# Performance work log

Measured on AMD Instinct MI355X. Metric: run time of the kernel, lower is better.

Reference implementation:

```python
import jax, jax.numpy as jnp
import numpy as np

B, DIM, H, W = 4, 96, 256, 256
HEADS = 4
EPS = 1e-12

def conv1x1(x, w, b):
    # x: [b,c,h,w], w: [o,c,1,1], b: [o]
    return jnp.einsum('bchw,oc->bohw', x, w[:, :, 0, 0]) + b[None, :, None, None]

def dwconv3x3(x, w, b):
    # depthwise 3x3, w: [c,1,3,3]
    c = x.shape[1]
    y = jax.lax.conv_general_dilated(
        x, w, window_strides=(1, 1), padding='SAME',
        feature_group_count=c, dimension_numbers=('NCHW', 'OIHW', 'NCHW'))
    return y + b[None, :, None, None]

def setup_inputs() -> dict:
    key = jax.random.key(0)
    ks = jax.random.split(key, 16)
    d = DIM
    s = 0.05
    return {
        'content': jax.random.normal(ks[0], (B, d, H, W), jnp.float32),
        'style': jax.random.normal(ks[1], (B, d, H, W), jnp.float32),
        'temperature': jnp.ones((HEADS, 1, 1), jnp.float32),
        'q_w': jax.random.normal(ks[2], (d, d, 1, 1), jnp.float32) * s,
        'q_b': jax.random.normal(ks[3], (d,), jnp.float32) * s,
        'qd_w': jax.random.normal(ks[4], (d, 1, 3, 3), jnp.float32) * s,
        'qd_b': jax.random.normal(ks[5], (d,), jnp.float32) * s,
        'kv_w': jax.random.normal(ks[6], (3 * d, d, 1, 1), jnp.float32) * s,
        'kv_b': jax.random.normal(ks[7], (3 * d,), jnp.float32) * s,
        'kvd_w': jax.random.normal(ks[8], (3 * d, 1, 3, 3), jnp.float32) * s,
        'kvd_b': jax.random.normal(ks[9], (3 * d,), jnp.float32) * s,
        'ps_w': jax.random.normal(ks[10], (d, d, 1, 1), jnp.float32) * s,
        'ps_b': jax.random.normal(ks[11], (d,), jnp.float32) * s,
        'psh_w': jax.random.normal(ks[12], (d, d, 1, 1), jnp.float32) * s,
        'psh_b': jax.random.normal(ks[13], (d,), jnp.float32) * s,
    }

def _heads(x, b, h, w):
    # [b, head*c, h, w] -> [b, head, c, h*w]
    return x.reshape(b, HEADS, x.shape[1] // HEADS, h * w)

def reference(content, style, temperature, q_w, q_b, qd_w, qd_b,
              kv_w, kv_b, kvd_w, kvd_b, ps_w, ps_b, psh_w, psh_b):
    b, c, h, w = content.shape
    kv = dwconv3x3(conv1x1(style, kv_w, kv_b), kvd_w, kvd_b)
    k, v_scale, v_shift = jnp.split(kv, 3, axis=1)
    q = dwconv3x3(conv1x1(content, q_w, q_b), qd_w, qd_b)

    q = _heads(q, b, h, w)
    k = _heads(k, b, h, w)
    v_scale = _heads(v_scale, b, h, w)
    v_shift = _heads(v_shift, b, h, w)

    # L2-normalize over spatial dim (torch F.normalize eps=1e-12)
    q = q / jnp.maximum(jnp.linalg.norm(q, axis=-1, keepdims=True), EPS)
    k = k / jnp.maximum(jnp.linalg.norm(k, axis=-1, keepdims=True), EPS)

    # attn: [b, head, c, c] (channel attention, tiny)
    attn = jnp.einsum('bhcn,bhdn->bhcd', q, k) * temperature[None]
    attn = jax.nn.softmax(attn, axis=-1)

    scale = jnp.einsum('bhcd,bhdn->bhcn', attn, v_scale).reshape(b, c, h, w)
    shift = jnp.einsum('bhcd,bhdn->bhcn', attn, v_shift).reshape(b, c, h, w)

    scale = conv1x1(scale, ps_w, ps_b)
    shift = conv1x1(shift, psh_w, psh_b)
    return (scale, shift)
```

## Files before the change

### kernel.cpp

```cpp
#include <hip/hip_runtime.h>

#define NB 4
#define C 96
#define HH 256
#define WW 256
#define NPIX (HH*WW)
#define HEADS 4
#define CH 24

#define NTX2 16
#define NTY2 19
#define NTILES (NTX2*NTY2)
#define YP 296
#define QP 264
#define VP 104
#define KSPLIT 128
#define YR 24
#define YC 392
#define XTP 76

#define WS_SUMSQ_Q 0
#define WS_SUMSQ_K (WS_SUMSQ_Q + NB*C)
#define WS_GRAM    (WS_SUMSQ_K + NB*C)
#define WS_MS      (WS_GRAM + NB*HEADS*CH*CH)
#define WS_MSH     (WS_MS + NB*C*C)

#define XT_OFF_BYTES ((size_t)335872)
#define XT_BYTES   ((size_t)2*NB*NPIX*96*2)

#define F_PSQ_OFF   (XT_OFF_BYTES + XT_BYTES)
#define F_PSQ_BYTES ((size_t)NTILES*NB*192*4)
#define F_PG_OFF    (F_PSQ_OFF + F_PSQ_BYTES)
#define F_PG_BYTES  ((size_t)NTILES*NB*HEADS*1024*4)
#define F_MB_OFF    (F_PG_OFF + F_PG_BYTES)
#define F_MB_BYTES  ((size_t)2*NB*96*96*2)
#define F_WS_NEED   (F_MB_OFF + F_MB_BYTES)

#define QK_OFF    (XT_OFF_BYTES + XT_BYTES)
#define QK_BYTES  ((size_t)2*NB*96*NPIX*2)
#define VB_OFF    (QK_OFF + QK_BYTES)
#define VB_BYTES  ((size_t)NB*NPIX*96*2)
#define PG_OFF    (VB_OFF + VB_BYTES)
#define PG_BYTES  ((size_t)KSPLIT*NB*9216*4)
#define PSQ_OFF   (PG_OFF + PG_BYTES)
#define PSQ_BYTES ((size_t)4*NTILES*NB*48*4)
#define MB_OFF    (PSQ_OFF + PSQ_BYTES)
#define MB_BYTES  ((size_t)2*NB*96*96*2)
#define WB_OFF    (MB_OFF + MB_BYTES)
#define WB_BYTES  ((size_t)384*96*2)
#define WS_NEED2  (WB_OFF + WB_BYTES)

typedef short short8 __attribute__((ext_vector_type(8)));
typedef float f32x4 __attribute__((ext_vector_type(4)));
typedef float f32x16 __attribute__((ext_vector_type(16)));

__device__ __forceinline__ unsigned short f2b(float f){
  unsigned u = __float_as_uint(f);
  unsigned r = u + 0x7FFFu + ((u >> 16) & 1u);
  return (unsigned short)(r >> 16);
}
__device__ __forceinline__ float b2f(unsigned short s){
  return __uint_as_float(((unsigned)s) << 16);
}
__device__ __forceinline__ short8 pack8(float4 a, float4 b){
  short8 r;
  r[0]=(short)f2b(a.x); r[1]=(short)f2b(a.y); r[2]=(short)f2b(a.z); r[3]=(short)f2b(a.w);
  r[4]=(short)f2b(b.x); r[5]=(short)f2b(b.y); r[6]=(short)f2b(b.z); r[7]=(short)f2b(b.w);
  return r;
}

__global__ __launch_bounds__(256) void k0t(
  const float* __restrict__ content, const float* __restrict__ style,
  unsigned short* __restrict__ xt, int cm)
{
  __shared__ unsigned short Xt[96*XTP];
  const int t = threadIdx.x;
  const int n0 = blockIdx.x * 64;
  const int b = blockIdx.y, src = blockIdx.z;
  const int gyr = n0 >> 8, gxb = n0 & 255;
  const float* in = (src ? style : content) + (size_t)b*C*NPIX;
  #pragma unroll
  for (int i = 0; i < 6; ++i){
    int s = i*256 + t;
    int r = s >> 4, c4 = s & 15;
    float4 f = *(const float4*)(in + (size_t)r*NPIX + n0 + c4*4);
    unsigned lo = ((unsigned)f2b(f.y) << 16) | f2b(f.x);
    unsigned hi = ((unsigned)f2b(f.w) << 16) | f2b(f.z);
    *(uint2*)&Xt[r*XTP + c4*4] = make_uint2(lo, hi);
  }
  __syncthreads();
  unsigned* dst = (unsigned*)(xt + ((size_t)src*NB + b)*NPIX*96);
  #pragma unroll
  for (int i = 0; i < 12; ++i){
    int s = i*256 + t;
    int j = s / 48, c2 = s - j*48;
    unsigned v = ((unsigned)Xt[(c2*2+1)*XTP + j] << 16) | Xt[(c2*2)*XTP + j];
    size_t np = cm ? ((size_t)(gxb + j)*HH + gyr) : (size_t)(n0 + j);
    dst[np*48 + c2] = v;
  }
}

__global__ __launch_bounds__(256) void kwpack(
  const float* __restrict__ q_w, const float* __restrict__ kv_w,
  unsigned short* __restrict__ wb)
{
  int i = blockIdx.x*256 + threadIdx.x;
  if (i < 9216) wb[i] = f2b(q_w[i]);
  else if (i < 36864) wb[i] = f2b(kv_w[i - 9216]);
}

__global__ __launch_bounds__(512, 4) void kconv(
  const unsigned short* __restrict__ xt, const unsigned short* __restrict__ wb,
  const float* __restrict__ q_b, const float* __restrict__ qd_w, const float* __restrict__ qd_b,
  const float* __restrict__ kv_b, const float* __restrict__ kvd_w, const float* __restrict__ kvd_b,
  unsigned short* __restrict__ qk, unsigned short* __restrict__ vbs,
  unsigned short* __restrict__ vbh, float* __restrict__ psq)
{
  __shared__ unsigned short Ysh[48*YC];
  __shared__ float red[48];
  const int t = threadIdx.x, lane = t & 63, w = t >> 6;
  const int tile = blockIdx.x, b = blockIdx.y, z = blockIdx.z;
  const int txx = tile & 15, tyy = tile >> 4;
  const int gx0 = txx*16, gy0 = tyy*14;
  const unsigned short* xsrc = xt + ((size_t)((z < 2 ? 0 : 1)*NB + b))*NPIX*96;
  const int wrow0 = (z < 2) ? z*48 : 96 + (z-2)*48;
  const float* cb  = (z<2) ? q_b  + z*48           : kv_b  + (size_t)(z-2)*48;
  const float* dww = (z<2) ? qd_w + (size_t)z*48*9 : kvd_w + (size_t)(z-2)*48*9;
  const float* dwb = (z<2) ? qd_b + z*48           : kvd_b + (size_t)(z-2)*48;
  unsigned short* dst0;
  if (z < 2)      dst0 = qk  + ((size_t)(0*NB + b)*96 + (size_t)z*48)*NPIX;
  else if (z < 4) dst0 = qk  + ((size_t)(1*NB + b)*96 + (size_t)(z-2)*48)*NPIX;
  else if (z < 6) dst0 = vbs + ((size_t)b*96 + (size_t)(z-4)*48)*NPIX;
  else            dst0 = vbh + ((size_t)b*96 + (size_t)(z-6)*48)*NPIX;

  if (t < 48) red[t] = 0.f;

  const int hy = lane & 15, khalf = lane >> 4;
  const int gyh = gy0 - 1 + hy;
  short8 xf[3][3]; bool imv[3];
  const int np = (w < 2) ? 3 : 2;
  #pragma unroll
  for (int i = 0; i < 3; ++i){
    if (i >= np) break;
    int pt = w + i*8;
    int gx = gx0 - 1 + pt;
    bool im = (gx>=0) && (gx<WW) && (gyh>=0) && (gyh<HH);
    imv[i] = im;
    const unsigned short* xp = xsrc + (size_t)(im ? (gx*HH + gyh) : 0)*96 + khalf*8;
    short8 zz = {};
    #pragma unroll
    for (int kk = 0; kk < 3; ++kk){
      short8 v = *(const short8*)(xp + kk*32);
      xf[i][kk] = im ? v : zz;
    }
  }

  #pragma unroll 1
  for (int mi = 0; mi < 3; ++mi){
    const unsigned short* wp = wb + (size_t)(wrow0 + mi*16 + hy)*96 + khalf*8;
    short8 a0 = *(const short8*)(wp);
    short8 a1 = *(const short8*)(wp + 32);
    short8 a2 = *(const short8*)(wp + 64);
    float4 bv = *(const float4*)&cb[mi*16 + khalf*4];
    #pragma unroll
    for (int i = 0; i < 3; ++i){
      if (i >= np) break;
      int pt = w + i*8;
      f32x4 acc = {bv.x, bv.y, bv.z, bv.w};
      acc = __builtin_amdgcn_mfma_f32_16x16x32_bf16(a0, xf[i][0], acc, 0,0,0);
      acc = __builtin_amdgcn_mfma_f32_16x16x32_bf16(a1, xf[i][1], acc, 0,0,0);
      acc = __builtin_amdgcn_mfma_f32_16x16x32_bf16(a2, xf[i][2], acc, 0,0,0);
      #pragma unroll
      for (int r = 0; r < 4; ++r){
        int ch = mi*16 + khalf*4 + r;
        Ysh[ch*YC + hy*YR + pt] = imv[i] ? f2b(acc[r]) : (unsigned short)0;
      }
    }
  }
  __syncthreads();

  for (int sl = lane; sl < 84; sl += 64){
    int slot = w*84 + sl;
    int c = slot / 14, py = slot - (slot/14)*14;
    int gy = gy0 + py;
    if (gy < HH){
      const float* wd = dww + (size_t)c*9;
      float w00=wd[0],w01=wd[1],w02=wd[2],w10=wd[3],w11=wd[4],w12=wd[5],w20=wd[6],w21=wd[7],w22=wd[8];
      float bb = dwb[c];
      const unsigned short* yb = &Ysh[c*YC + py*YR];
      float o[16];
      #pragma unroll
      for (int half = 0; half < 2; ++half){
        float u[3][10];
        #pragma unroll
        for (int uu = 0; uu < 3; ++uu){
          const unsigned short* rp = yb + uu*YR + half*8;
          short8 s = *(const short8*)rp;
          unsigned ex = *(const unsigned*)(rp + 8);
          #pragma unroll
          for (int j = 0; j < 8; ++j) u[uu][j] = b2f((unsigned short)s[j]);
          u[uu][8] = b2f((unsigned short)(ex & 0xffffu));
          u[uu][9] = b2f((unsigned short)(ex >> 16));
        }
        #pragma unroll
        for (int j = 0; j < 8; ++j){
          float s = bb;
          s = fmaf(w00,u[0][j],s); s = fmaf(w01,u[0][j+1],s); s = fmaf(w02,u[0][j+2],s);
          s = fmaf(w10,u[1][j],s); s = fmaf(w11,u[1][j+1],s); s = fmaf(w12,u[1][j+2],s);
          s = fmaf(w20,u[2][j],s); s = fmaf(w21,u[2][j+1],s); s = fmaf(w22,u[2][j+2],s);
          o[half*8 + j] = s;
        }
      }
      unsigned short vv[16];
      if (z < 4){
        float sq = 0.f;
        #pragma unroll
        for (int j = 0; j < 16; ++j){ sq = fmaf(o[j], o[j], sq); vv[j] = f2b(o[j]); }
        atomicAdd(&red[c], sq);
      } else {
        #pragma unroll
        for (int j = 0; j < 16; ++j) vv[j] = f2b(o[j]);
      }
      unsigned short* qp = dst0 + (size_t)c*NPIX + (size_t)gy*WW + gx0;
      *(short8*)qp       = *(const short8*)&vv[0];
      *(short8*)(qp + 8) = *(const short8*)&vv[8];
    }
  }
  if (z < 4){
    __syncthreads();
    if (t < 48)
      psq[((size_t)(z*NTILES + tile)*NB + b)*48 + t] = red[t];
  }
}

__global__ __launch_bounds__(384) void kgram(
  const unsigned short* __restrict__ qk, float* __restrict__ pg)
{
  const int t = threadIdx.x, lane = t & 63, wv = t >> 6;
  const int ks = blockIdx.x, b = blockIdx.y;
  const int n0 = ks * (NPIX / KSPLIT);
  const unsigned short* qb = qk + ((size_t)(0*NB + b)*96)*NPIX;
  const unsigned short* kb = qk + ((size_t)(1*NB + b)*96)*NPIX;
  f32x4 acc[6];
  #pragma unroll
  for (int i = 0; i < 6; ++i) acc[i] = (f32x4){0.f,0.f,0.f,0.f};
  #pragma unroll 1
  for (int st = 0; st < (NPIX/KSPLIT)/32; ++st){
    int off = n0 + st*32 + (lane>>4)*8;
    short8 bf = *(const short8*)(kb + (size_t)(wv*16 + (lane&15))*NPIX + off);
    #pragma unroll
    for (int ci = 0; ci < 6; ++ci){
      short8 af = *(const short8*)(qb + (size_t)(ci*16 + (lane&15))*NPIX + off);
      acc[ci] = __builtin_amdgcn_mfma_f32_16x16x32_bf16(af, bf, acc[ci], 0,0,0);
    }
  }
  float* dst = pg + ((size_t)ks*NB + b)*9216;
  #pragma unroll
  for (int ci = 0; ci < 6; ++ci){
    #pragma unroll
    for (int r = 0; r < 4; ++r)
      dst[(ci*6 + wv)*256 + ((lane>>4)*4 + r)*16 + (lane&15)] = acc[ci][r];
  }
}

__global__ __launch_bounds__(256) void kgredN(
  const float* __restrict__ pg, const float* __restrict__ psq, float* __restrict__ ws)
{
  const int b = blockIdx.x, by = blockIdx.y, t = threadIdx.x;
  if (by < 36){
    int ci = by / 6;
    int qrow = ci*16 + (t >> 4), krow = (by - ci*6)*16 + (t & 15);
    float s = 0.f;
    for (int ks = 0; ks < KSPLIT; ++ks)
      s += pg[((size_t)ks*NB + b)*9216 + by*256 + t];
    int h = qrow / CH;
    if (krow / CH == h)
      ws[WS_GRAM + ((size_t)(b*HEADS + h)*CH + (qrow % CH))*CH + (krow % CH)] = s;
  } else {
    if (t < 192){
      int src = t / 96, c = t - (t/96)*96;
      int zz = src*2 + (c/48), cc = c - (c/48)*48;
      float s = 0.f;
      for (int tile = 0; tile < NTILES; ++tile)
        s += psq[((size_t)(zz*NTILES + tile)*NB + b)*48 + cc];
      ws[(src ? WS_SUMSQ_K : WS_SUMSQ_Q) + b*C + c] = s;
    }
  }
}

__global__ void k2_attn(
  const float* __restrict__ temp,
  const float* __restrict__ ps_w, const float* __restrict__ psh_w,
  float* __restrict__ ws, unsigned short* __restrict__ mb)
{
  const int b = blockIdx.x;
  const int t = threadIdx.x;
  __shared__ float attn[C * CH];
  __shared__ float nq[C], nk[C];
  if (t < C){
    nq[t] = fmaxf(sqrtf(ws[WS_SUMSQ_Q + b * C + t]), 1e-12f);
    nk[t] = fmaxf(sqrtf(ws[WS_SUMSQ_K + b * C + t]), 1e-12f);
  }
  __syncthreads();
  if (t < C){
    int h = t / CH;
    const float* g = ws + WS_GRAM + (((size_t)b * HEADS + h) * CH + (t % CH)) * CH;
    float tp = temp[h];
    float row[CH];
    float mx = -3.4e38f;
    #pragma unroll
    for (int d = 0; d < CH; ++d){
      row[d] = g[d] / (nq[t] * nk[h * CH + d]) * tp;
      mx = fmaxf(mx, row[d]);
    }
    float s = 0.f;
    #pragma unroll
    for (int d = 0; d < CH; ++d){ row[d] = expf(row[d] - mx); s += row[d]; }
    float inv = 1.f / s;
    #pragma unroll
    for (int d = 0; d < CH; ++d) attn[t * CH + d] = row[d] * inv;
  }
  __syncthreads();
  for (int idx = t; idx < C * C; idx += 256){
    int o = idx / C, dg = idx - o * C;
    int h = dg / CH, d = dg - h * CH;
    float s1 = 0.f, s2 = 0.f;
    #pragma unroll
    for (int c2 = 0; c2 < CH; ++c2){
      float a = attn[(h * CH + c2) * CH + d];
      s1 = fmaf(ps_w [(size_t)o * C + h * CH + c2], a, s1);
      s2 = fmaf(psh_w[(size_t)o * C + h * CH + c2], a, s2);
    }
    ws[WS_MS  + (size_t)b * C * C + idx] = s1;
    ws[WS_MSH + (size_t)b * C * C + idx] = s2;
    if (mb){
      mb[((size_t)0*NB + b)*9216 + idx] = f2b(s1);
      mb[((size_t)1*NB + b)*9216 + idx] = f2b(s2);
    }
  }
}

__global__ __launch_bounds__(512) void kMv(
  const unsigned short* __restrict__ vb, const unsigned short* __restrict__ mb,
  const float* __restrict__ bias, float* __restrict__ out)
{
  __shared__ unsigned short vS[256*VP + 32*8];
  unsigned* vS32 = (unsigned*)vS;
  const int t = threadIdx.x, lane = t & 63, w = t >> 6;
  const int b = blockIdx.y;
  const int n0 = blockIdx.x * 256;
  const unsigned short* vbase = vb + (size_t)b*96*NPIX;
  #pragma unroll
  for (int i = 0; i < 3; ++i){
    int task = i*512 + t;
    int cp = task >> 5, seg = task & 31;
    const unsigned short* r0 = vbase + (size_t)(2*cp)*NPIX + n0 + seg*8;
    short8 a  = *(const short8*)r0;
    short8 bq = *(const short8*)(r0 + NPIX);
    #pragma unroll
    for (int j = 0; j < 8; ++j){
      int px = seg*8 + j;
      unsigned d = ((unsigned)(unsigned short)bq[j] << 16) | (unsigned)(unsigned short)a[j];
      vS32[px*(VP/2) + (px>>3)*4 + cp] = d;
    }
  }
  __syncthreads();
  const unsigned short* mbb = mb + (size_t)b*9216;
  float* ob = out + (size_t)b*C*NPIX;
  #pragma unroll 1
  for (int mi = 0; mi < 6; ++mi){
    const unsigned short* mp = mbb + (size_t)(mi*16 + (lane & 15))*96 + (lane>>4)*8;
    short8 a0 = *(const short8*)(mp);
    short8 a1 = *(const short8*)(mp + 32);
    short8 a2 = *(const short8*)(mp + 64);
    float4 bv = *(const float4*)&bias[mi*16 + (lane>>4)*4];
    #pragma unroll
    for (int g = 0; g < 2; ++g){
      int px = (w*2 + g)*16 + (lane & 15);
      const unsigned short* xb = &vS[px*VP + (px>>3)*8 + (lane>>4)*8];
      f32x4 acc = {bv.x, bv.y, bv.z, bv.w};
      acc = __builtin_amdgcn_mfma_f32_16x16x32_bf16(a0, *(const short8*)(xb),    acc, 0,0,0);
      acc = __builtin_amdgcn_mfma_f32_16x16x32_bf16(a1, *(const short8*)(xb+32), acc, 0,0,0);
      acc = __builtin_amdgcn_mfma_f32_16x16x32_bf16(a2, *(const short8*)(xb+64), acc, 0,0,0);
      #pragma unroll
      for (int r = 0; r < 4; ++r)
        ob[(size_t)(mi*16 + (lane>>4)*4 + r)*NPIX + n0 + px] = acc[r];
    }
  }
}

__device__ __forceinline__ void conv48c(
  const unsigned short* __restrict__ xbase, const float* __restrict__ wmat,
  const float* __restrict__ bias, int row0,
  int gx0, int gy0, int lane, int w, unsigned short* __restrict__ Ysh)
{
  const int hy = lane & 15, khalf = lane >> 4;
  const int gy = gy0 - 1 + hy;
  short8 xf[3][3]; bool imv[3]; int np = (w < 2) ? 3 : 2;
  #pragma unroll
  for (int i = 0; i < 3; ++i){
    if (i >= np) break;
    int pt = w + i*8;
    int gx = gx0 - 1 + pt;
    bool im = (gx>=0) && (gx<WW) && (gy>=0) && (gy<HH);
    imv[i] = im;
    int n = im ? (gy*WW + gx) : 0;
    const unsigned short* xp = xbase + (size_t)n*96 + khalf*8;
    short8 z = {};
    #pragma unroll
    for (int kk = 0; kk < 3; ++kk){
      short8 v = *(const short8*)(xp + kk*32);
      xf[i][kk] = im ? v : z;
    }
  }
  #pragma unroll 1
  for (int mi = 0; mi < 3; ++mi){
    int orow = row0 + mi*16 + hy;
    const float* wp = wmat + (size_t)orow*96 + khalf*8;
    short8 a0 = pack8(*(const float4*)(wp),    *(const float4*)(wp+4));
    short8 a1 = pack8(*(const float4*)(wp+32), *(const float4*)(wp+36));
    short8 a2 = pack8(*(const float4*)(wp+64), *(const float4*)(wp+68));
    float4 bv = *(const float4*)&bias[row0 + mi*16 + khalf*4];
    #pragma unroll
    for (int i = 0; i < 3; ++i){
      if (i >= np) break;
      int pt = w + i*8;
      f32x4 acc = {bv.x, bv.y, bv.z, bv.w};
      acc = __builtin_amdgcn_mfma_f32_16x16x32_bf16(a0, xf[i][0], acc, 0,0,0);
      acc = __builtin_amdgcn_mfma_f32_16x16x32_bf16(a1, xf[i][1], acc, 0,0,0);
      acc = __builtin_amdgcn_mfma_f32_16x16x32_bf16(a2, xf[i][2], acc, 0,0,0);
      #pragma unroll
      for (int r = 0; r < 4; ++r){
        int ch = mi*16 + khalf*4 + r;
        Ysh[ch*YP + pt*16 + hy] = imv[i] ? f2b(acc[r]) : (unsigned short)0;
      }
    }
  }
}

__global__ __launch_bounds__(512, 4) void kqk(
  const unsigned short* __restrict__ xt,
  const float* __restrict__ q_w, const float* __restrict__ q_b,
  const float* __restrict__ qd_w, const float* __restrict__ qd_b,
  const float* __restrict__ kv_w, const float* __restrict__ kv_b,
  const float* __restrict__ kvd_w, const float* __restrict__ kvd_b,
  float* __restrict__ pg, float* __restrict__ psq)
{
  __shared__ unsigned short Ysh[48*YP];
  __shared__ unsigned short qS[48*QP];
  __shared__ unsigned short kT[48*QP];
  __shared__ float redq[C], redk[C];

  const int t = threadIdx.x, lane = t & 63, w = t >> 6;
  const int b = blockIdx.y, tile = blockIdx.x;
  const int txx = tile & 15, tyy = tile >> 4;
  const int gx0 = txx*16, gy0 = tyy*14;
  if (t < C){ redq[t] = 0.f; redk[t] = 0.f; }
  __syncthreads();

  const unsigned short* xc = xt + ((size_t)(0*NB + b))*NPIX*96;
  const unsigned short* xs = xt + ((size_t)(1*NB + b))*NPIX*96;

  auto dwQK = [&](const float* dww, const float* dwb, int wrow0,
                  unsigned short* dst, float* red){
    for (int slot = t; slot < 48*16; slot += 512){
      int c = slot >> 4, j = slot & 15;
      const unsigned short* yb = &Ysh[c*YP + j*16];
      float u0[16], u1[16], u2[16];
      {
        short8 s0 = *(const short8*)(yb),    s1 = *(const short8*)(yb+8);
        short8 s2 = *(const short8*)(yb+16), s3 = *(const short8*)(yb+24);
        short8 s4 = *(const short8*)(yb+32), s5 = *(const short8*)(yb+40);
        #pragma unroll
        for (int u = 0; u < 8; ++u){
          u0[u]=b2f((unsigned short)s0[u]); u0[u+8]=b2f((unsigned short)s1[u]);
          u1[u]=b2f((unsigned short)s2[u]); u1[u+8]=b2f((unsigned short)s3[u]);
          u2[u]=b2f((unsigned short)s4[u]); u2[u+8]=b2f((unsigned short)s5[u]);
        }
      }
      const float* wd = dww + (size_t)(wrow0 + c)*9;
      float w00=wd[0],w01=wd[1],w02=wd[2],w10=wd[3],w11=wd[4],w12=wd[5],w20=wd[6],w21=wd[7],w22=wd[8];
      float bb = dwb[wrow0 + c];
      unsigned short vv[16];
      float sq = 0.f;
      #pragma unroll
      for (int py = 0; py < 14; ++py){
        float s = bb;
        s = fmaf(w00,u0[py],s); s = fmaf(w10,u0[py+1],s); s = fmaf(w20,u0[py+2],s);
        s = fmaf(w01,u1[py],s); s = fmaf(w11,u1[py+1],s); s = fmaf(w21,u1[py+2],s);
        s = fmaf(w02,u2[py],s); s = fmaf(w12,u2[py+1],s); s = fmaf(w22,u2[py+2],s);
        if (gy0 + py >= HH) s = 0.f;
        sq = fmaf(s, s, sq);
        vv[py] = f2b(s);
      }
      vv[14] = 0; vv[15] = 0;
      atomicAdd(&red[wrow0 + c], sq);
      *(short8*)&dst[c*QP + j*16]     = *(short8*)&vv[0];
      *(short8*)&dst[c*QP + j*16 + 8] = *(short8*)&vv[8];
    }
  };

  auto gram = [&](int cc){
    int hl = w & 1, slice = w >> 1;
    int cl = lane & 31; bool cv = cl < CH;
    int row = hl*CH + (cv ? cl : 0);
    f32x16 g;
    #pragma unroll
    for (int r = 0; r < 16; ++r) g[r] = 0.f;
    short8 z = {};
    for (int ks = slice; ks < 16; ks += 4){
      int ko = ks*16 + (lane>>5)*8;
      short8 qa = *(const short8*)&qS[row*QP + ko];
      short8 kb = *(const short8*)&kT[row*QP + ko];
      if (!cv){ qa = z; kb = z; }
      g = __builtin_amdgcn_mfma_f32_32x32x16_bf16(qa, kb, g, 0,0,0);
    }
    float* stg = (float*)Ysh;
    if (slice != 0){
      float* dst = stg + (size_t)(hl*3 + slice - 1)*1024;
      #pragma unroll
      for (int r = 0; r < 16; ++r) dst[r*64 + lane] = g[r];
    }
    __syncthreads();
    if (slice == 0){
      const float* s0 = stg + (size_t)(hl*3 + 0)*1024;
      const float* s1 = stg + (size_t)(hl*3 + 1)*1024;
      const float* s2 = stg + (size_t)(hl*3 + 2)*1024;
      float* dst = pg + ((size_t)(tile*NB + b)*HEADS + cc*2 + hl)*1024;
      #pragma unroll
      for (int r = 0; r < 16; ++r){
        int ix = r*64 + lane;
        dst[ix] = g[r] + s0[ix] + s1[ix] + s2[ix];
      }
    }
  };

  #pragma unroll 1
  for (int cc = 0; cc < 2; ++cc){
    conv48c(xc, q_w, q_b, cc*48, gx0, gy0, lane, w, Ysh);
    __syncthreads();
    dwQK(qd_w, qd_b, cc*48, qS, redq);
    __syncthreads();
    conv48c(xs, kv_w, kv_b, cc*48, gx0, gy0, lane, w, Ysh);
    __syncthreads();
    dwQK(kvd_w, kvd_b, cc*48, kT, redk);
    __syncthreads();
    gram(cc);
    __syncthreads();
  }
  if (t < 192){
    float v = (t < 96) ? redq[t] : redk[t - 96];
    psq[(size_t)(tile*NB + b)*192 + t] = v;
  }
}

__global__ __launch_bounds__(256) void kgredF(
  const float* __restrict__ pg, const float* __restrict__ psq, float* __restrict__ ws)
{
  const int bh = blockIdx.x;
  const int b = bh >> 2, h = bh & 3;
  const int t = threadIdx.x;
  float a0=0.f, a1=0.f, a2=0.f, a3=0.f, sq=0.f;
  for (int tile = 0; tile < NTILES; ++tile){
    const float* p = pg + ((size_t)(tile*NB + b)*HEADS + h)*1024;
    a0 += p[t]; a1 += p[t+256]; a2 += p[t+512]; a3 += p[t+768];
    if (t < 48){
      int ch = h*CH + (t % CH);
      sq += psq[(size_t)(tile*NB + b)*192 + (t < CH ? ch : 96 + ch)];
    }
  }
  if (t < 48){
    if (t < CH) ws[WS_SUMSQ_Q + b*C + h*CH + t] = sq;
    else        ws[WS_SUMSQ_K + b*C + h*CH + (t - CH)] = sq;
  }
  float accs[4] = {a0, a1, a2, a3};
  #pragma unroll
  for (int i = 0; i < 4; ++i){
    int idx = i*256 + t;
    int r = idx >> 6, ln = idx & 63;
    int row = (r&3) + 8*(r>>2) + 4*(ln>>5);
    int col = ln & 31;
    if (row < CH && col < CH)
      ws[WS_GRAM + ((size_t)(b*HEADS + h)*CH + row)*CH + col] = accs[i];
  }
}

__global__ __launch_bounds__(512, 4) void kv_out(
  const unsigned short* __restrict__ xs,
  const float* __restrict__ kv_w, const float* __restrict__ kv_b,
  const float* __restrict__ kvd_w, const float* __restrict__ kvd_b,
  const float* __restrict__ ps_b, const float* __restrict__ psh_b,
  const unsigned short* __restrict__ mb, float* __restrict__ out)
{
  __shared__ unsigned short Ysh[48*YP];
  __shared__ unsigned short vS2[224*VP];
  const int t = threadIdx.x, lane = t & 63, w = t >> 6;
  const int b = blockIdx.y, tile = blockIdx.x;
  const int txx = tile & 15, tyy = tile >> 4;
  const int gx0 = txx*16, gy0 = tyy*14;
  const unsigned short* xb_ = xs + (size_t)b*NPIX*96;

  #pragma unroll 1
  for (int which = 0; which < 2; ++which){
    #pragma unroll 1
    for (int cv = 0; cv < 2; ++cv){
      int row0 = 96 + which*96 + cv*48;
      conv48c(xb_, kv_w, kv_b, row0, gx0, gy0, lane, w, Ysh);
      __syncthreads();
      for (int slot = t; slot < 48*16; slot += 512){
        int c = slot >> 4, j = slot & 15;
        const unsigned short* yb = &Ysh[c*YP + j*16];
        float u0[16], u1[16], u2[16];
        {
          short8 s0 = *(const short8*)(yb),    s1 = *(const short8*)(yb+8);
          short8 s2 = *(const short8*)(yb+16), s3 = *(const short8*)(yb+24);
          short8 s4 = *(const short8*)(yb+32), s5 = *(const short8*)(yb+40);
          #pragma unroll
          for (int u = 0; u < 8; ++u){
            u0[u]=b2f((unsigned short)s0[u]); u0[u+8]=b2f((unsigned short)s1[u]);
            u1[u]=b2f((unsigned short)s2[u]); u1[u+8]=b2f((unsigned short)s3[u]);
            u2[u]=b2f((unsigned short)s4[u]); u2[u+8]=b2f((unsigned short)s5[u]);
          }
        }
        const float* wd = kvd_w + (size_t)(row0 + c)*9;
        float w00=wd[0],w01=wd[1],w02=wd[2],w10=wd[3],w11=wd[4],w12=wd[5],w20=wd[6],w21=wd[7],w22=wd[8];
        float bb = kvd_b[row0 + c];
        #pragma unroll
        for (int py = 0; py < 14; ++py){
          float s = bb;
          s = fmaf(w00,u0[py],s); s = fmaf(w10,u0[py+1],s); s = fmaf(w20,u0[py+2],s);
          s = fmaf(w01,u1[py],s); s = fmaf(w11,u1[py+1],s); s = fmaf(w21,u1[py+2],s);
          s = fmaf(w02,u2[py],s); s = fmaf(w12,u2[py+1],s); s = fmaf(w22,u2[py+2],s);
          vS2[(py*16 + j)*VP + cv*48 + c] = f2b(s);
        }
      }
      __syncthreads();
    }
    const unsigned short* mbp = mb + ((size_t)which*NB + b)*9216;
    const float* bias = which ? psh_b : ps_b;
    float* ob = out + (size_t)which*NB*C*NPIX + (size_t)b*C*NPIX;
    for (int tl = w; tl < 84; tl += 8){
      int mi = tl / 14, n = tl - mi*14;
      const unsigned short* mp = mbp + (size_t)(mi*16 + (lane&15))*96 + (lane>>4)*8;
      short8 a0 = *(const short8*)(mp);
      short8 a1 = *(const short8*)(mp + 32);
      short8 a2 = *(const short8*)(mp + 64);
      float4 bv = *(const float4*)&bias[mi*16 + (lane>>4)*4];
      f32x4 acc = {bv.x, bv.y, bv.z, bv.w};
      const unsigned short* xb = &vS2[(size_t)(n*16 + (lane&15))*VP + (lane>>4)*8];
      acc = __builtin_amdgcn_mfma_f32_16x16x32_bf16(a0, *(const short8*)(xb),    acc, 0,0,0);
      acc = __builtin_amdgcn_mfma_f32_16x16x32_bf16(a1, *(const short8*)(xb+32), acc, 0,0,0);
      acc = __builtin_amdgcn_mfma_f32_16x16x32_bf16(a2, *(const short8*)(xb+64), acc, 0,0,0);
      int gy = gy0 + n;
      if (gy < HH){
        #pragma unroll
        for (int r = 0; r < 4; ++r)
          ob[(size_t)(mi*16 + (lane>>4)*4 + r)*NPIX + gy*WW + gx0 + (lane&15)] = acc[r];
      }
    }
    __syncthreads();
  }
}

extern "C" void kernel_launch(void* const* d_in, const int* in_sizes, int n_in,
                              void* d_out, int out_size, void* d_ws, size_t ws_size,
                              hipStream_t stream)
{
  const float* content = (const float*)d_in[0];
  const float* style   = (const float*)d_in[1];
  const float* temp    = (const float*)d_in[2];
  const float* q_w   = (const float*)d_in[3];
  const float* q_b   = (const float*)d_in[4];
  const float* qd_w  = (const float*)d_in[5];
  const float* qd_b  = (const float*)d_in[6];
  const float* kv_w  = (const float*)d_in[7];
  const float* kv_b  = (const float*)d_in[8];
  const float* kvd_w = (const float*)d_in[9];
  const float* kvd_b = (const float*)d_in[10];
  const float* ps_w  = (const float*)d_in[11];
  const float* ps_b  = (const float*)d_in[12];
  const float* psh_w = (const float*)d_in[13];
  const float* psh_b = (const float*)d_in[14];
  float* out = (float*)d_out;
  float* ws  = (float*)d_ws;

  unsigned short* xt = (unsigned short*)((char*)d_ws + XT_OFF_BYTES);

  if (ws_size >= WS_NEED2){
    unsigned short* qk  = (unsigned short*)((char*)d_ws + QK_OFF);
    unsigned short* vbh = (unsigned short*)((char*)d_ws + VB_OFF);
    unsigned short* vbs = (unsigned short*)(out + (size_t)NB*C*NPIX);
    float* pg  = (float*)((char*)d_ws + PG_OFF);
    float* psq = (float*)((char*)d_ws + PSQ_OFF);
    unsigned short* mb = (unsigned short*)((char*)d_ws + MB_OFF);
    unsigned short* wb = (unsigned short*)((char*)d_ws + WB_OFF);

    k0t<<<dim3(NPIX/64, NB, 2), dim3(256), 0, stream>>>(content, style, xt, 1);
    kwpack<<<dim3(144), dim3(256), 0, stream>>>(q_w, kv_w, wb);
    kconv<<<dim3(NTILES, NB, 8), dim3(512), 0, stream>>>(
        xt, wb, q_b, qd_w, qd_b, kv_b, kvd_w, kvd_b, qk, vbs, vbh, psq);
    kgram<<<dim3(KSPLIT, NB), dim3(384), 0, stream>>>(qk, pg);
    kgredN<<<dim3(NB, 37), dim3(256), 0, stream>>>(pg, psq, ws);
    k2_attn<<<dim3(NB), dim3(256), 0, stream>>>(temp, ps_w, psh_w, ws, mb);
    kMv<<<dim3(NPIX/256, NB), dim3(512), 0, stream>>>(vbs, mb, ps_b, out);
    kMv<<<dim3(NPIX/256, NB), dim3(512), 0, stream>>>(
        vbh, mb + (size_t)NB*9216, psh_b, out + (size_t)NB*C*NPIX);
  } else {
    float* pg  = (float*)((char*)d_ws + F_PG_OFF);
    float* psq = (float*)((char*)d_ws + F_PSQ_OFF);
    unsigned short* mb = (unsigned short*)((char*)d_ws + F_MB_OFF);
    k0t<<<dim3(NPIX/64, NB, 2), dim3(256), 0, stream>>>(content, style, xt, 0);
    kqk<<<dim3(NTILES, NB), dim3(512), 0, stream>>>(
        xt, q_w, q_b, qd_w, qd_b, kv_w, kv_b, kvd_w, kvd_b, pg, psq);
    kgredF<<<dim3(NB*HEADS), dim3(256), 0, stream>>>(pg, psq, ws);
    k2_attn<<<dim3(NB), dim3(256), 0, stream>>>(temp, ps_w, psh_w, ws, mb);
    kv_out<<<dim3(NTILES, NB), dim3(512), 0, stream>>>(
        xt + (size_t)NB*NPIX*96, kv_w, kv_b, kvd_w, kvd_b, ps_b, psh_b, mb, out);
  }
}
```

Before: 436.8 us.

## Fuse V-branch conv recompute with attention-mix output GEMM, drop V intermediates

```diff
diff --git a/kernel.cpp b/kernel.cpp
--- a/kernel.cpp
+++ b/kernel.cpp
@@ -18,6 +18,7 @@
 #define YR 24
 #define YC 392
 #define XTP 76
+#define VCH 40
 
 #define WS_SUMSQ_Q 0
 #define WS_SUMSQ_K (WS_SUMSQ_Q + NB*C)
@@ -38,9 +39,7 @@
 
 #define QK_OFF    (XT_OFF_BYTES + XT_BYTES)
 #define QK_BYTES  ((size_t)2*NB*96*NPIX*2)
-#define VB_OFF    (QK_OFF + QK_BYTES)
-#define VB_BYTES  ((size_t)NB*NPIX*96*2)
-#define PG_OFF    (VB_OFF + VB_BYTES)
+#define PG_OFF    (QK_OFF + QK_BYTES)
 #define PG_BYTES  ((size_t)KSPLIT*NB*9216*4)
 #define PSQ_OFF   (PG_OFF + PG_BYTES)
 #define PSQ_BYTES ((size_t)4*NTILES*NB*48*4)
@@ -48,7 +47,7 @@
 #define MB_BYTES  ((size_t)2*NB*96*96*2)
 #define WB_OFF    (MB_OFF + MB_BYTES)
 #define WB_BYTES  ((size_t)384*96*2)
-#define WS_NEED2  (WB_OFF + WB_BYTES)
+#define WS_NEED3  (WB_OFF + WB_BYTES)
 
 typedef short short8 __attribute__((ext_vector_type(8)));
 typedef float f32x4 __attribute__((ext_vector_type(4)));
@@ -61,6 +60,11 @@
 }
 __device__ __forceinline__ float b2f(unsigned short s){
   return __uint_as_float(((unsigned)s) << 16);
+}
+__device__ __forceinline__ unsigned cvtpk(float lo, float hi){
+  unsigned r;
+  asm("v_cvt_pk_bf16_f32 %0, %1, %2" : "=v"(r) : "v"(lo), "v"(hi));
+  return r;
 }
 __device__ __forceinline__ short8 pack8(float4 a, float4 b){
   short8 r;
@@ -113,8 +117,7 @@
   const unsigned short* __restrict__ xt, const unsigned short* __restrict__ wb,
   const float* __restrict__ q_b, const float* __restrict__ qd_w, const float* __restrict__ qd_b,
   const float* __restrict__ kv_b, const float* __restrict__ kvd_w, const float* __restrict__ kvd_b,
-  unsigned short* __restrict__ qk, unsigned short* __restrict__ vbs,
-  unsigned short* __restrict__ vbh, float* __restrict__ psq)
+  unsigned short* __restrict__ qk, float* __restrict__ psq)
 {
   __shared__ unsigned short Ysh[48*YC];
   __shared__ float red[48];
@@ -127,11 +130,9 @@
   const float* cb  = (z<2) ? q_b  + z*48           : kv_b  + (size_t)(z-2)*48;
   const float* dww = (z<2) ? qd_w + (size_t)z*48*9 : kvd_w + (size_t)(z-2)*48*9;
   const float* dwb = (z<2) ? qd_b + z*48           : kvd_b + (size_t)(z-2)*48;
-  unsigned short* dst0;
-  if (z < 2)      dst0 = qk  + ((size_t)(0*NB + b)*96 + (size_t)z*48)*NPIX;
-  else if (z < 4) dst0 = qk  + ((size_t)(1*NB + b)*96 + (size_t)(z-2)*48)*NPIX;
-  else if (z < 6) dst0 = vbs + ((size_t)b*96 + (size_t)(z-4)*48)*NPIX;
-  else            dst0 = vbh + ((size_t)b*96 + (size_t)(z-6)*48)*NPIX;
+  unsigned short* dst0 = (z < 2)
+      ? qk + ((size_t)(0*NB + b)*96 + (size_t)z*48)*NPIX
+      : qk + ((size_t)(1*NB + b)*96 + (size_t)(z-2)*48)*NPIX;
 
   if (t < 48) red[t] = 0.f;
 
@@ -211,26 +212,21 @@
           o[half*8 + j] = s;
         }
       }
-      unsigned short vv[16];
-      if (z < 4){
-        float sq = 0.f;
-        #pragma unroll
-        for (int j = 0; j < 16; ++j){ sq = fmaf(o[j], o[j], sq); vv[j] = f2b(o[j]); }
-        atomicAdd(&red[c], sq);
-      } else {
-        #pragma unroll
-        for (int j = 0; j < 16; ++j) vv[j] = f2b(o[j]);
-      }
+      float sq = 0.f;
+      #pragma unroll
+      for (int j = 0; j < 16; ++j) sq = fmaf(o[j], o[j], sq);
+      atomicAdd(&red[c], sq);
+      unsigned vvp[8];
+      #pragma unroll
+      for (int jj = 0; jj < 8; ++jj) vvp[jj] = cvtpk(o[2*jj], o[2*jj+1]);
       unsigned short* qp = dst0 + (size_t)c*NPIX + (size_t)gy*WW + gx0;
-      *(short8*)qp       = *(const short8*)&vv[0];
-      *(short8*)(qp + 8) = *(const short8*)&vv[8];
-    }
-  }
-  if (z < 4){
-    __syncthreads();
-    if (t < 48)
-      psq[((size_t)(z*NTILES + tile)*NB + b)*48 + t] = red[t];
-  }
+      *(uint4*)qp       = make_uint4(vvp[0], vvp[1], vvp[2], vvp[3]);
+      *(uint4*)(qp + 8) = make_uint4(vvp[4], vvp[5], vvp[6], vvp[7]);
+    }
+  }
+  __syncthreads();
+  if (t < 48)
+    psq[((size_t)(z*NTILES + tile)*NB + b)*48 + t] = red[t];
 }
 
 __global__ __launch_bounds__(384) void kgram(
@@ -340,51 +336,141 @@
   }
 }
 
-__global__ __launch_bounds__(512) void kMv(
-  const unsigned short* __restrict__ vb, const unsigned short* __restrict__ mb,
-  const float* __restrict__ bias, float* __restrict__ out)
-{
-  __shared__ unsigned short vS[256*VP + 32*8];
-  unsigned* vS32 = (unsigned*)vS;
+__global__ __launch_bounds__(512, 4) void kvm(
+  const unsigned short* __restrict__ xt, const unsigned short* __restrict__ wb,
+  const float* __restrict__ kv_b, const float* __restrict__ kvd_w, const float* __restrict__ kvd_b,
+  const unsigned short* __restrict__ mb,
+  const float* __restrict__ ps_b, const float* __restrict__ psh_b,
+  float* __restrict__ out)
+{
+  __shared__ unsigned short Ysh[32*YC];
+  __shared__ unsigned short vS[224*VCH];
   const int t = threadIdx.x, lane = t & 63, w = t >> 6;
-  const int b = blockIdx.y;
-  const int n0 = blockIdx.x * 256;
-  const unsigned short* vbase = vb + (size_t)b*96*NPIX;
+  const int tile = blockIdx.x, b = blockIdx.y, z = blockIdx.z;
+  const int txx = tile & 15, tyy = tile >> 4;
+  const int gx0 = txx*16, gy0 = tyy*14;
+  const unsigned short* xsrc = xt + ((size_t)(NB + b))*NPIX*96;
+
+  const int hy = lane & 15, khalf = lane >> 4;
+  const int gyh = gy0 - 1 + hy;
+  short8 xf[3][3]; bool imv[3];
+  const int np = (w < 2) ? 3 : 2;
   #pragma unroll
   for (int i = 0; i < 3; ++i){
-    int task = i*512 + t;
-    int cp = task >> 5, seg = task & 31;
-    const unsigned short* r0 = vbase + (size_t)(2*cp)*NPIX + n0 + seg*8;
-    short8 a  = *(const short8*)r0;
-    short8 bq = *(const short8*)(r0 + NPIX);
-    #pragma unroll
-    for (int j = 0; j < 8; ++j){
-      int px = seg*8 + j;
-      unsigned d = ((unsigned)(unsigned short)bq[j] << 16) | (unsigned)(unsigned short)a[j];
-      vS32[px*(VP/2) + (px>>3)*4 + cp] = d;
-    }
-  }
-  __syncthreads();
-  const unsigned short* mbb = mb + (size_t)b*9216;
-  float* ob = out + (size_t)b*C*NPIX;
+    if (i >= np) break;
+    int pt = w + i*8;
+    int gx = gx0 - 1 + pt;
+    bool im = (gx>=0) && (gx<WW) && (gyh>=0) && (gyh<HH);
+    imv[i] = im;
+    const unsigned short* xp = xsrc + (size_t)(im ? (gx*HH + gyh) : 0)*96 + khalf*8;
+    short8 zz = {};
+    #pragma unroll
+    for (int kk = 0; kk < 3; ++kk){
+      short8 v = *(const short8*)(xp + kk*32);
+      xf[i][kk] = im ? v : zz;
+    }
+  }
+
+  const float* bias = z ? psh_b : ps_b;
+  f32x4 acc[6][2];
+  #pragma unroll
+  for (int mi = 0; mi < 6; ++mi){
+    float4 bv = *(const float4*)&bias[mi*16 + khalf*4];
+    acc[mi][0] = (f32x4){bv.x, bv.y, bv.z, bv.w};
+    acc[mi][1] = acc[mi][0];
+  }
+  const unsigned short* mbp = mb + ((size_t)z*NB + b)*9216;
+
   #pragma unroll 1
-  for (int mi = 0; mi < 6; ++mi){
-    const unsigned short* mp = mbb + (size_t)(mi*16 + (lane & 15))*96 + (lane>>4)*8;
-    short8 a0 = *(const short8*)(mp);
-    short8 a1 = *(const short8*)(mp + 32);
-    short8 a2 = *(const short8*)(mp + 64);
-    float4 bv = *(const float4*)&bias[mi*16 + (lane>>4)*4];
-    #pragma unroll
-    for (int g = 0; g < 2; ++g){
-      int px = (w*2 + g)*16 + (lane & 15);
-      const unsigned short* xb = &vS[px*VP + (px>>3)*8 + (lane>>4)*8];
-      f32x4 acc = {bv.x, bv.y, bv.z, bv.w};
-      acc = __builtin_amdgcn_mfma_f32_16x16x32_bf16(a0, *(const short8*)(xb),    acc, 0,0,0);
-      acc = __builtin_amdgcn_mfma_f32_16x16x32_bf16(a1, *(const short8*)(xb+32), acc, 0,0,0);
-      acc = __builtin_amdgcn_mfma_f32_16x16x32_bf16(a2, *(const short8*)(xb+64), acc, 0,0,0);
-      #pragma unroll
-      for (int r = 0; r < 4; ++r)
-        ob[(size_t)(mi*16 + (lane>>4)*4 + r)*NPIX + n0 + px] = acc[r];
+  for (int ck = 0; ck < 3; ++ck){
+    const int kvrow0 = 96 + z*96 + ck*32;
+    #pragma unroll 1
+    for (int mi2 = 0; mi2 < 2; ++mi2){
+      const unsigned short* wp = wb + (size_t)(96 + kvrow0 + mi2*16 + hy)*96 + khalf*8;
+      short8 a0 = *(const short8*)(wp);
+      short8 a1 = *(const short8*)(wp + 32);
+      short8 a2 = *(const short8*)(wp + 64);
+      float4 bv = *(const float4*)&kv_b[kvrow0 + mi2*16 + khalf*4];
+      #pragma unroll
+      for (int i = 0; i < 3; ++i){
+        if (i >= np) break;
+        int pt = w + i*8;
+        f32x4 a = {bv.x, bv.y, bv.z, bv.w};
+        a = __builtin_amdgcn_mfma_f32_16x16x32_bf16(a0, xf[i][0], a, 0,0,0);
+        a = __builtin_amdgcn_mfma_f32_16x16x32_bf16(a1, xf[i][1], a, 0,0,0);
+        a = __builtin_amdgcn_mfma_f32_16x16x32_bf16(a2, xf[i][2], a, 0,0,0);
+        #pragma unroll
+        for (int r = 0; r < 4; ++r){
+          int ch = mi2*16 + khalf*4 + r;
+          Ysh[ch*YC + hy*YR + pt] = imv[i] ? f2b(a[r]) : (unsigned short)0;
+        }
+      }
+    }
+    __syncthreads();
+    if (t < 448){
+      int c2 = t & 31, py = t >> 5;
+      const float* wd = kvd_w + (size_t)(kvrow0 + c2)*9;
+      float w00=wd[0],w01=wd[1],w02=wd[2],w10=wd[3],w11=wd[4],w12=wd[5],w20=wd[6],w21=wd[7],w22=wd[8];
+      float bb = kvd_b[kvrow0 + c2];
+      const unsigned short* yb = &Ysh[c2*YC + py*YR];
+      float o[16];
+      #pragma unroll
+      for (int half = 0; half < 2; ++half){
+        float u[3][10];
+        #pragma unroll
+        for (int uu = 0; uu < 3; ++uu){
+          const unsigned short* rp = yb + uu*YR + half*8;
+          short8 s = *(const short8*)rp;
+          unsigned ex = *(const unsigned*)(rp + 8);
+          #pragma unroll
+          for (int j = 0; j < 8; ++j) u[uu][j] = b2f((unsigned short)s[j]);
+          u[uu][8] = b2f((unsigned short)(ex & 0xffffu));
+          u[uu][9] = b2f((unsigned short)(ex >> 16));
+        }
+        #pragma unroll
+        for (int j = 0; j < 8; ++j){
+          float s = bb;
+          s = fmaf(w00,u[0][j],s); s = fmaf(w01,u[0][j+1],s); s = fmaf(w02,u[0][j+2],s);
+          s = fmaf(w10,u[1][j],s); s = fmaf(w11,u[1][j+1],s); s = fmaf(w12,u[1][j+2],s);
+          s = fmaf(w20,u[2][j],s); s = fmaf(w21,u[2][j+1],s); s = fmaf(w22,u[2][j+2],s);
+          o[half*8 + j] = s;
+        }
+      }
+      #pragma unroll
+      for (int jj = 0; jj < 8; ++jj){
+        unsigned p = cvtpk(o[2*jj], o[2*jj+1]);
+        vS[(py*16 + 2*jj    )*VCH + c2] = (unsigned short)p;
+        vS[(py*16 + 2*jj + 1)*VCH + c2] = (unsigned short)(p >> 16);
+      }
+    }
+    __syncthreads();
+    #pragma unroll
+    for (int mi = 0; mi < 6; ++mi){
+      short8 a = *(const short8*)(mbp + (size_t)(mi*16 + hy)*96 + ck*32 + khalf*8);
+      #pragma unroll
+      for (int gi = 0; gi < 2; ++gi){
+        int g = w + gi*8;
+        if (g < 14){
+          short8 bf = *(const short8*)&vS[(size_t)(g*16 + hy)*VCH + khalf*8];
+          acc[mi][gi] = __builtin_amdgcn_mfma_f32_16x16x32_bf16(a, bf, acc[mi][gi], 0,0,0);
+        }
+      }
+    }
+    __syncthreads();
+  }
+
+  float* ob = out + ((size_t)z*NB + b)*(size_t)C*NPIX;
+  #pragma unroll
+  for (int gi = 0; gi < 2; ++gi){
+    int g = w + gi*8;
+    int gy = gy0 + g;
+    if (g < 14 && gy < HH){
+      #pragma unroll
+      for (int mi = 0; mi < 6; ++mi){
+        #pragma unroll
+        for (int r = 0; r < 4; ++r)
+          ob[(size_t)(mi*16 + khalf*4 + r)*NPIX + (size_t)gy*WW + gx0 + hy] = acc[mi][gi][r];
+      }
     }
   }
 }
@@ -468,9 +554,11 @@
       const unsigned short* yb = &Ysh[c*YP + j*16];
       float u0[16], u1[16], u2[16];
       {
-        short8 s0 = *(const short8*)(yb),    s1 = *(const short8*)(yb+8);
+        short8 s0 = *(const short8*)(yb),    short8_t_dummy = {};
+        short8 s1 = *(const short8*)(yb+8);
         short8 s2 = *(const short8*)(yb+16), s3 = *(const short8*)(yb+24);
         short8 s4 = *(const short8*)(yb+32), s5 = *(const short8*)(yb+40);
+        (void)short8_t_dummy;
         #pragma unroll
         for (int u = 0; u < 8; ++u){
           u0[u]=b2f((unsigned short)s0[u]); u0[u+8]=b2f((unsigned short)s1[u]);
@@ -686,10 +774,8 @@
 
   unsigned short* xt = (unsigned short*)((char*)d_ws + XT_OFF_BYTES);
 
-  if (ws_size >= WS_NEED2){
+  if (ws_size >= WS_NEED3){
     unsigned short* qk  = (unsigned short*)((char*)d_ws + QK_OFF);
-    unsigned short* vbh = (unsigned short*)((char*)d_ws + VB_OFF);
-    unsigned short* vbs = (unsigned short*)(out + (size_t)NB*C*NPIX);
     float* pg  = (float*)((char*)d_ws + PG_OFF);
     float* psq = (float*)((char*)d_ws + PSQ_OFF);
     unsigned short* mb = (unsigned short*)((char*)d_ws + MB_OFF);
@@ -697,14 +783,13 @@
 
     k0t<<<dim3(NPIX/64, NB, 2), dim3(256), 0, stream>>>(content, style, xt, 1);
     kwpack<<<dim3(144), dim3(256), 0, stream>>>(q_w, kv_w, wb);
-    kconv<<<dim3(NTILES, NB, 8), dim3(512), 0, stream>>>(
-        xt, wb, q_b, qd_w, qd_b, kv_b, kvd_w, kvd_b, qk, vbs, vbh, psq);
+    kconv<<<dim3(NTILES, NB, 4), dim3(512), 0, stream>>>(
+        xt, wb, q_b, qd_w, qd_b, kv_b, kvd_w, kvd_b, qk, psq);
     kgram<<<dim3(KSPLIT, NB), dim3(384), 0, stream>>>(qk, pg);
     kgredN<<<dim3(NB, 37), dim3(256), 0, stream>>>(pg, psq, ws);
     k2_attn<<<dim3(NB), dim3(256), 0, stream>>>(temp, ps_w, psh_w, ws, mb);
-    kMv<<<dim3(NPIX/256, NB), dim3(512), 0, stream>>>(vbs, mb, ps_b, out);
-    kMv<<<dim3(NPIX/256, NB), dim3(512), 0, stream>>>(
-        vbh, mb + (size_t)NB*9216, psh_b, out + (size_t)NB*C*NPIX);
+    kvm<<<dim3(NTILES, NB, 2), dim3(512), 0, stream>>>(
+        xt, wb, kv_b, kvd_w, kvd_b, mb, ps_b, psh_b, out);
   } else {
     float* pg  = (float*)((char*)d_ws + F_PG_OFF);
     float* psq = (float*)((char*)d_ws + F_PSQ_OFF);
```

After: 449.1 us. 1.03x slower.
